# Kernel optimization log

Hardware: AMD Instinct MI355X
Metric: run time of the kernel (lower is better)

Reference implementation:

```python
import jax, jax.numpy as jnp
import numpy as np

B, T = 256, 512
V, H, L, O = 29275, 128, 2, 3


def setup_inputs() -> dict:
    key = jax.random.key(0)
    ks = jax.random.split(key, 8)
    s_emb = 1.0  # torch nn.Embedding default init is N(0,1)
    s = 1.0 / np.sqrt(H)  # torch GRU/Linear default U(-1/sqrt(H), 1/sqrt(H))
    return {
        "x": jax.random.randint(ks[0], (B, T), 0, V, dtype=jnp.int32),
        "emb": jax.random.normal(ks[1], (V, H), dtype=jnp.float32) * s_emb,
        "W_ih": jax.random.uniform(ks[2], (L, 3 * H, H), jnp.float32, -s, s),
        "W_hh": jax.random.uniform(ks[3], (L, 3 * H, H), jnp.float32, -s, s),
        "b_ih": jax.random.uniform(ks[4], (L, 3 * H), jnp.float32, -s, s),
        "b_hh": jax.random.uniform(ks[5], (L, 3 * H), jnp.float32, -s, s),
        "fc_w": jax.random.uniform(ks[6], (O, H), jnp.float32, -s, s),
        "fc_b": jax.random.uniform(ks[7], (O,), jnp.float32, -s, s),
    }


def _gru_layer(inp, Wih, Whh, bih, bhh):
    # inp: [B, T, H]. PyTorch GRU gate order: r, z, n.
    gx = jnp.einsum("bth,gh->btg", inp, Wih) + bih  # [B, T, 3H] input-side gates

    def step(h, gx_t):
        gh = h @ Whh.T + bhh  # [B, 3H]
        xr, xz, xn = jnp.split(gx_t, 3, axis=-1)
        hr, hz, hn = jnp.split(gh, 3, axis=-1)
        r = jax.nn.sigmoid(xr + hr)
        z = jax.nn.sigmoid(xz + hz)
        n = jnp.tanh(xn + r * hn)
        h_new = (1.0 - z) * n + z * h
        return h_new, h_new

    h0 = jnp.zeros((inp.shape[0], Whh.shape[1]), dtype=inp.dtype)
    _, outs = jax.lax.scan(step, h0, gx.transpose(1, 0, 2))  # [T, B, H]
    return outs.transpose(1, 0, 2)


def reference(x, emb, W_ih, W_hh, b_ih, b_hh, fc_w, fc_b):
    h = emb[x]  # [B, T, H] embedding lookup
    for l in range(L):  # small fixed layer count; dropout inactive in eval mode
        h = _gru_layer(h, W_ih[l], W_hh[l], b_ih[l], b_hh[l])
    last = jax.nn.relu(h[:, -1])  # [B, H]
    return last @ fc_w.T + fc_b  # [B, O]
```

## Files before the change

kernel.cpp:

```cpp
#include <hip/hip_runtime.h>
#include <hip/hip_bf16.h>

#define B_   256
#define T_   512
#define H_   128
#define G3_  384

#define TM   128
#define TN   128
#define TK   32
#define LDA  132

#define LOG2E_F  1.4426950408889634f
#define LOG2E2_F 2.8853900817779268f

typedef float v4f __attribute__((ext_vector_type(4)));
typedef float v2f __attribute__((ext_vector_type(2)));

__device__ __forceinline__ float fast_rcp(float x) {
    return __builtin_amdgcn_rcpf(x);
}
__device__ __forceinline__ float exp2_raw(float x) {
    return __builtin_amdgcn_exp2f(x);
}

__device__ __forceinline__ void pk_fma(v2f& acc, v2f a, v2f b) {
    asm("v_pk_fma_f32 %0, %1, %2, %0" : "+v"(acc) : "v"(a), "v"(b));
}

__device__ __forceinline__ float bfly_fold4(float v) {
    int x;
    x = __builtin_amdgcn_update_dpp(0, __float_as_int(v), 0x0B1, 0xF, 0xF, true);
    v += __int_as_float(x);
    x = __builtin_amdgcn_update_dpp(0, __float_as_int(v), 0x04E, 0xF, 0xF, true);
    v += __int_as_float(x);
    return v;
}

__device__ __forceinline__ void lds_barrier() {
    asm volatile("s_waitcnt lgkmcnt(0)" ::: "memory");
    __builtin_amdgcn_s_barrier();
    asm volatile("" ::: "memory");
}

template<bool GATHER>
__global__ __launch_bounds__(256, 2)
void gx_gemm(const float* __restrict__ X,
             const int*   __restrict__ idx,
             const float* __restrict__ emb,
             const float* __restrict__ W,
             const float* __restrict__ bias,
             const float* __restrict__ bias2,
             float*       __restrict__ gx)
{
    __shared__ __align__(16) float As[2][TK][LDA];
    __shared__ __align__(16) float Bs[2][TK][LDA];

    const int tid = threadIdx.x;
    const int tn  = tid & 15;
    const int tm  = tid >> 4;
    const int n0  = blockIdx.x * TN;
    const int m0  = blockIdx.y * TM;

    const int q  = tid & 7;
    const float* rowA[4];
    const float* rowB[4];
#pragma unroll
    for (int s = 0; s < 4; s++) {
        const int r = (tid >> 3) + 32 * s;
        rowA[s] = GATHER ? (emb + (size_t)idx[m0 + r] * H_)
                         : (X + (size_t)(m0 + r) * H_);
        rowB[s] = W + (size_t)(n0 + r) * H_;
    }

    float4 stA[4], stB[4];
    auto load_chunk = [&](int kc) {
#pragma unroll
        for (int s = 0; s < 4; s++) {
            stA[s] = *(const float4*)(rowA[s] + kc + q * 4);
            stB[s] = *(const float4*)(rowB[s] + kc + q * 4);
        }
    };
    auto store_chunk = [&](int buf) {
#pragma unroll
        for (int s = 0; s < 4; s++) {
            const int r = (tid >> 3) + 32 * s;
#pragma unroll
            for (int d = 0; d < 4; d++) {
                As[buf][q * 4 + d][r] = ((const float*)&stA[s])[d];
                Bs[buf][q * 4 + d][r] = ((const float*)&stB[s])[d];
            }
        }
    };

    float4 acc[2][2][4];
#pragma unroll
    for (int a = 0; a < 2; a++)
#pragma unroll
        for (int b = 0; b < 2; b++)
#pragma unroll
            for (int c = 0; c < 4; c++) acc[a][b][c] = make_float4(0.f, 0.f, 0.f, 0.f);

    load_chunk(0);
    store_chunk(0);
    __syncthreads();

    for (int c = 0; c < 4; c++) {
        if (c < 3) load_chunk((c + 1) * TK);
        const int buf = c & 1;
#pragma unroll 4
        for (int k = 0; k < TK; k++) {
            float4 a0 = *(const float4*)&As[buf][k][tm * 4];
            float4 a1 = *(const float4*)&As[buf][k][64 + tm * 4];
            float4 b0 = *(const float4*)&Bs[buf][k][tn * 4];
            float4 b1 = *(const float4*)&Bs[buf][k][64 + tn * 4];
            float4 av[2] = {a0, a1}, bv[2] = {b0, b1};
#pragma unroll
            for (int mg = 0; mg < 2; mg++)
#pragma unroll
                for (int mi = 0; mi < 4; mi++) {
                    const float am = ((const float*)&av[mg])[mi];
#pragma unroll
                    for (int ng = 0; ng < 2; ng++) {
                        acc[mg][ng][mi].x = fmaf(am, bv[ng].x, acc[mg][ng][mi].x);
                        acc[mg][ng][mi].y = fmaf(am, bv[ng].y, acc[mg][ng][mi].y);
                        acc[mg][ng][mi].z = fmaf(am, bv[ng].z, acc[mg][ng][mi].z);
                        acc[mg][ng][mi].w = fmaf(am, bv[ng].w, acc[mg][ng][mi].w);
                    }
                }
        }
        if (c < 3) {
            store_chunk(buf ^ 1);
            __syncthreads();
        }
    }

    float4 bb0 = *(const float4*)(bias + n0 + tn * 4);
    float4 bb1 = *(const float4*)(bias + n0 + 64 + tn * 4);
    if (n0 < 2 * H_) {
        const float4 c0 = *(const float4*)(bias2 + n0 + tn * 4);
        const float4 c1 = *(const float4*)(bias2 + n0 + 64 + tn * 4);
        bb0.x += c0.x; bb0.y += c0.y; bb0.z += c0.z; bb0.w += c0.w;
        bb1.x += c1.x; bb1.y += c1.y; bb1.z += c1.z; bb1.w += c1.w;
    }
    const float esc = (n0 < 2 * H_) ? LOG2E_F : LOG2E2_F;
#pragma unroll
    for (int mg = 0; mg < 2; mg++)
#pragma unroll
        for (int mi = 0; mi < 4; mi++) {
            const int m = m0 + mg * 64 + tm * 4 + mi;
            float* dst = gx + (size_t)m * G3_ + n0;
            float4 v0 = acc[mg][0][mi];
            v0.x = (v0.x + bb0.x) * esc; v0.y = (v0.y + bb0.y) * esc;
            v0.z = (v0.z + bb0.z) * esc; v0.w = (v0.w + bb0.w) * esc;
            float4 v1 = acc[mg][1][mi];
            v1.x = (v1.x + bb1.x) * esc; v1.y = (v1.y + bb1.y) * esc;
            v1.z = (v1.z + bb1.z) * esc; v1.w = (v1.w + bb1.w) * esc;
            *(float4*)(dst + tn * 4) = v0;
            *(float4*)(dst + 64 + tn * 4) = v1;
        }
}

template<bool STORE_H, bool FINAL>
__global__ __launch_bounds__(512)
__attribute__((amdgpu_waves_per_eu(2, 2)))
void gru_rec(const float* __restrict__ gx,
             const float* __restrict__ Whh,
             const float* __restrict__ bhh,
             float*       __restrict__ hseq,
             const float* __restrict__ fc_w,
             const float* __restrict__ fc_b,
             float*       __restrict__ out)
{
    __shared__ __align__(16) float h2[2][H_];

    const int tid = threadIdx.x;
    const int b   = blockIdx.x;
    const int jg  = tid >> 2;
    const int ks  = tid & 3;

    v2f Wr[16], Wz[16], Wn[16];
    {
        const v4f* wr = (const v4f*)(Whh + (size_t)(jg      ) * H_ + ks * 32);
        const v4f* wz = (const v4f*)(Whh + (size_t)(jg + 128) * H_ + ks * 32);
        const v4f* wn = (const v4f*)(Whh + (size_t)(jg + 256) * H_ + ks * 32);
#pragma unroll
        for (int c = 0; c < 8; c++) {
            v4f t;
            t = wr[c] * LOG2E_F;  Wr[2 * c] = t.lo; Wr[2 * c + 1] = t.hi;
            t = wz[c] * LOG2E_F;  Wz[2 * c] = t.lo; Wz[2 * c + 1] = t.hi;
            t = wn[c] * LOG2E2_F; Wn[2 * c] = t.lo; Wn[2 * c + 1] = t.hi;
        }
    }

    const float bhn = bhh[jg + 2 * H_] * LOG2E2_F;

    const float* gxb = gx + (size_t)b * T_ * G3_;
    float gr = gxb[jg], gz = gxb[jg + 128], gn = gxb[jg + 256];
    float h_old = 0.0f;

    if (tid < H_) h2[0][tid] = 0.0f;

    const int hw = ((jg >> 2) & 7) * 16 + (jg >> 5) * 4 + (jg & 3);
    const int hb = ks * 4;

    const float* gnx = gxb + G3_;
    float* hp = STORE_H ? (hseq + (size_t)b * T_ * H_ + jg) : nullptr;

    __syncthreads();

#define GRU_STEP(HIN, HOUT)                                                   \
    {                                                                         \
        const float gr2_ = gnx[jg];                                           \
        const float gz2_ = gnx[jg + 128];                                     \
        const float gn2_ = gnx[jg + 256];                                     \
        gnx += G3_;                                                           \
        v2f pr = {0.f, 0.f}, pz = {0.f, 0.f}, pn = {0.f, 0.f};                \
        _Pragma("unroll")                                                     \
        for (int c = 0; c < 8; c++) {                                         \
            v4f hv = *(const v4f*)&(HIN)[16 * c + hb];                        \
            v2f hlo = hv.lo, hhi = hv.hi;                                     \
            pk_fma(pr, hlo, Wr[2 * c]);  pk_fma(pr, hhi, Wr[2 * c + 1]);      \
            pk_fma(pz, hlo, Wz[2 * c]);  pk_fma(pz, hhi, Wz[2 * c + 1]);      \
            pk_fma(pn, hlo, Wn[2 * c]);  pk_fma(pn, hhi, Wn[2 * c + 1]);      \
        }                                                                     \
        const float p0 = bfly_fold4(pr.x + pr.y);                             \
        const float p1 = bfly_fold4(pz.x + pz.y);                             \
        const float p2 = bfly_fold4(pn.x + pn.y);                             \
        const float r_ = fast_rcp(1.0f + exp2_raw(-(gr + p0)));               \
        const float z_ = fast_rcp(1.0f + exp2_raw(-(gz + p1)));               \
        const float n_ = fmaf(-2.0f,                                          \
            fast_rcp(exp2_raw(gn + r_ * (p2 + bhn)) + 1.0f), 1.0f);           \
        h_old = fmaf(z_, h_old - n_, n_);                                     \
        if (ks == 0) {                                                        \
            (HOUT)[hw] = h_old;                                               \
            if (STORE_H) *hp = h_old;                                         \
        }                                                                     \
        if (STORE_H) hp += H_;                                                \
        gr = gr2_; gz = gz2_; gn = gn2_;                                      \
        lds_barrier();                                                        \
    }

    for (int t = 0; t < T_; t += 2) {
        GRU_STEP(h2[0], h2[1])
        GRU_STEP(h2[1], h2[0])
    }
#undef GRU_STEP

    if (FINAL) {
        if (ks == 0) h2[1][jg] = fmaxf(h_old, 0.0f);
        __syncthreads();
        if (tid < 3) {
            float acc = fc_b[tid];
            const float* fw = fc_w + tid * H_;
#pragma unroll
            for (int k = 0; k < H_; k++) acc = fmaf(h2[1][k], fw[k], acc);
            out[b * 3 + tid] = acc;
        }
    }
}

extern "C" void kernel_launch(void* const* d_in, const int* in_sizes, int n_in,
                              void* d_out, int out_size, void* d_ws, size_t ws_size,
                              hipStream_t stream)
{
    const int*   x    = (const int*)  d_in[0];
    const float* emb  = (const float*)d_in[1];
    const float* W_ih = (const float*)d_in[2];
    const float* W_hh = (const float*)d_in[3];
    const float* b_ih = (const float*)d_in[4];
    const float* b_hh = (const float*)d_in[5];
    const float* fc_w = (const float*)d_in[6];
    const float* fc_b = (const float*)d_in[7];
    float* out = (float*)d_out;

    const int M = B_ * T_;
    const size_t gx_f32 = (size_t)M * G3_ * sizeof(float);

    float* gx = (float*)d_ws;
    float* h1 = (float*)((char*)d_ws + gx_f32);

    dim3 ggx(G3_ / TN, M / TM);
    dim3 bgx(256);
    dim3 grec(B_), brec(512);

    hipLaunchKernelGGL((gx_gemm<true>), ggx, bgx, 0, stream,
                       nullptr, x, emb, W_ih, b_ih, b_hh, gx);
    hipLaunchKernelGGL((gru_rec<true, false>), grec, brec, 0, stream,
                       gx, W_hh, b_hh, h1, nullptr, nullptr, nullptr);
    hipLaunchKernelGGL((gx_gemm<false>), ggx, bgx, 0, stream,
                       h1, nullptr, nullptr, W_ih + G3_ * H_, b_ih + G3_,
                       b_hh + G3_, gx);
    hipLaunchKernelGGL((gru_rec<false, true>), grec, brec, 0, stream,
                       gx, W_hh + G3_ * H_, b_hh + G3_, nullptr, fc_w, fc_b, out);
}
```

Measured before the change: 882.2 us.

## Fuse layer-2 input projection into layer-1 recurrence using extra warps

Replaces the layer-1 recurrence kernel and the layer-2 input GEMM with a single 1024-thread kernel. Half the threads run the layer-1 recurrence, and the other half compute the layer-2 input gates from the shared hidden state one step behind, writing them back into the gx buffer in place. This removes the h1 sequence round trip through global memory and one kernel launch. The cost is doubled block size and register pressure, plus per-step barriers over twice as many waves, which may slow the serial recurrence.

```diff
diff --git a/kernel.cpp b/kernel.cpp
--- a/kernel.cpp
+++ b/kernel.cpp
@@ -159,6 +159,150 @@
             *(float4*)(dst + tn * 4) = v0;
             *(float4*)(dst + 64 + tn * 4) = v1;
         }
+}
+
+__global__ __launch_bounds__(1024)
+__attribute__((amdgpu_waves_per_eu(4, 4)))
+void gru_fused(float*       __restrict__ gx,
+               const float* __restrict__ Whh,
+               const float* __restrict__ bhh,
+               const float* __restrict__ Wih2,
+               const float* __restrict__ bih2,
+               const float* __restrict__ bhh2)
+{
+    __shared__ __align__(16) float h2[2][H_];
+
+    const int tid = threadIdx.x;
+    const int b   = blockIdx.x;
+    float* gxb = gx + (size_t)b * T_ * G3_;
+
+    if (tid < H_) h2[0][tid] = 0.0f;
+    __syncthreads();
+
+    if (tid < 512) {
+        const int jg = tid >> 2;
+        const int ks = tid & 3;
+
+        v2f Wr[16], Wz[16], Wn[16];
+        {
+            const v4f* wr = (const v4f*)(Whh + (size_t)(jg      ) * H_ + ks * 32);
+            const v4f* wz = (const v4f*)(Whh + (size_t)(jg + 128) * H_ + ks * 32);
+            const v4f* wn = (const v4f*)(Whh + (size_t)(jg + 256) * H_ + ks * 32);
+#pragma unroll
+            for (int c = 0; c < 8; c++) {
+                v4f t;
+                t = wr[c] * LOG2E_F;  Wr[2 * c] = t.lo; Wr[2 * c + 1] = t.hi;
+                t = wz[c] * LOG2E_F;  Wz[2 * c] = t.lo; Wz[2 * c + 1] = t.hi;
+                t = wn[c] * LOG2E2_F; Wn[2 * c] = t.lo; Wn[2 * c + 1] = t.hi;
+            }
+        }
+
+        const float bhn = bhh[jg + 2 * H_] * LOG2E2_F;
+        float gr = gxb[jg], gz = gxb[jg + 128], gn = gxb[jg + 256];
+        float h_old = 0.0f;
+
+        const int hw = ((jg >> 2) & 7) * 16 + (jg >> 5) * 4 + (jg & 3);
+        const int hb = ks * 4;
+        const float* gnx = gxb + G3_;
+
+#define REC_STEP(HIN, HOUT)                                                   \
+        {                                                                     \
+            const float gr2_ = gnx[jg];                                       \
+            const float gz2_ = gnx[jg + 128];                                 \
+            const float gn2_ = gnx[jg + 256];                                 \
+            gnx += G3_;                                                       \
+            v2f pr = {0.f, 0.f}, pz = {0.f, 0.f}, pn = {0.f, 0.f};            \
+            _Pragma("unroll")                                                 \
+            for (int c = 0; c < 8; c++) {                                     \
+                v4f hv = *(const v4f*)&(HIN)[16 * c + hb];                    \
+                v2f hlo = hv.lo, hhi = hv.hi;                                 \
+                pk_fma(pr, hlo, Wr[2 * c]);  pk_fma(pr, hhi, Wr[2 * c + 1]);  \
+                pk_fma(pz, hlo, Wz[2 * c]);  pk_fma(pz, hhi, Wz[2 * c + 1]);  \
+                pk_fma(pn, hlo, Wn[2 * c]);  pk_fma(pn, hhi, Wn[2 * c + 1]);  \
+            }                                                                 \
+            const float p0 = bfly_fold4(pr.x + pr.y);                         \
+            const float p1 = bfly_fold4(pz.x + pz.y);                         \
+            const float p2 = bfly_fold4(pn.x + pn.y);                         \
+            const float r_ = fast_rcp(1.0f + exp2_raw(-(gr + p0)));           \
+            const float z_ = fast_rcp(1.0f + exp2_raw(-(gz + p1)));           \
+            const float n_ = fmaf(-2.0f,                                      \
+                fast_rcp(exp2_raw(gn + r_ * (p2 + bhn)) + 1.0f), 1.0f);       \
+            h_old = fmaf(z_, h_old - n_, n_);                                 \
+            if (ks == 0) (HOUT)[hw] = h_old;                                  \
+            gr = gr2_; gz = gz2_; gn = gn2_;                                  \
+            lds_barrier();                                                    \
+        }
+
+        for (int t = 0; t < T_; t += 2) {
+            REC_STEP(h2[0], h2[1])
+            REC_STEP(h2[1], h2[0])
+        }
+#undef REC_STEP
+    } else {
+        const int t2 = tid - 512;
+        const int jq = t2 >> 2;
+        const int kq = t2 & 3;
+
+        v2f Ar[16], Az[16], An[16];
+        {
+            const v4f* ar = (const v4f*)(Wih2 + (size_t)(jq      ) * H_ + kq * 32);
+            const v4f* az = (const v4f*)(Wih2 + (size_t)(jq + 128) * H_ + kq * 32);
+            const v4f* an = (const v4f*)(Wih2 + (size_t)(jq + 256) * H_ + kq * 32);
+#pragma unroll
+            for (int c = 0; c < 8; c++) {
+                v4f t;
+                t = ar[c] * LOG2E_F;  Ar[2 * c] = t.lo; Ar[2 * c + 1] = t.hi;
+                t = az[c] * LOG2E_F;  Az[2 * c] = t.lo; Az[2 * c + 1] = t.hi;
+                t = an[c] * LOG2E2_F; An[2 * c] = t.lo; An[2 * c + 1] = t.hi;
+            }
+        }
+
+        const float br2 = (bih2[jq]          + bhh2[jq])          * LOG2E_F;
+        const float bz2 = (bih2[jq + H_]     + bhh2[jq + H_])     * LOG2E_F;
+        const float bn2 =  bih2[jq + 2 * H_]                      * LOG2E2_F;
+
+        const int qb   = kq * 4;
+        const int woff = jq + (kq - 1) * H_;
+        float* gxw = gxb - G3_;
+
+#define Q_DOT(HIN)                                                            \
+            v2f qr = {0.f, 0.f}, qz = {0.f, 0.f}, qn = {0.f, 0.f};            \
+            _Pragma("unroll")                                                 \
+            for (int c = 0; c < 8; c++) {                                     \
+                v4f hv = *(const v4f*)&(HIN)[16 * c + qb];                    \
+                v2f hlo = hv.lo, hhi = hv.hi;                                 \
+                pk_fma(qr, hlo, Ar[2 * c]);  pk_fma(qr, hhi, Ar[2 * c + 1]);  \
+                pk_fma(qz, hlo, Az[2 * c]);  pk_fma(qz, hhi, Az[2 * c + 1]);  \
+                pk_fma(qn, hlo, An[2 * c]);  pk_fma(qn, hhi, An[2 * c + 1]);  \
+            }                                                                 \
+            const float q0 = bfly_fold4(qr.x + qr.y) + br2;                   \
+            const float q1 = bfly_fold4(qz.x + qz.y) + bz2;                   \
+            const float q2 = bfly_fold4(qn.x + qn.y) + bn2;
+
+#define Q_STEP(HIN, TT)                                                       \
+        {                                                                     \
+            Q_DOT(HIN)                                                        \
+            if ((TT) > 0 && kq != 0) {                                        \
+                gxw[woff] = (kq == 1) ? q0 : ((kq == 2) ? q1 : q2);           \
+            }                                                                 \
+            gxw += G3_;                                                       \
+            lds_barrier();                                                    \
+        }
+
+        for (int t = 0; t < T_; t += 2) {
+            Q_STEP(h2[0], t)
+            Q_STEP(h2[1], t + 1)
+        }
+
+        {
+            Q_DOT(h2[0])
+            if (kq != 0) {
+                gxw[woff] = (kq == 1) ? q0 : ((kq == 2) ? q1 : q2);
+            }
+        }
+#undef Q_STEP
+#undef Q_DOT
+    }
 }
 
 template<bool STORE_H, bool FINAL>
@@ -275,22 +419,18 @@
     float* out = (float*)d_out;
 
     const int M = B_ * T_;
-    const size_t gx_f32 = (size_t)M * G3_ * sizeof(float);
 
     float* gx = (float*)d_ws;
-    float* h1 = (float*)((char*)d_ws + gx_f32);
 
     dim3 ggx(G3_ / TN, M / TM);
     dim3 bgx(256);
-    dim3 grec(B_), brec(512);
+    dim3 grec(B_);
 
     hipLaunchKernelGGL((gx_gemm<true>), ggx, bgx, 0, stream,
                        nullptr, x, emb, W_ih, b_ih, b_hh, gx);
-    hipLaunchKernelGGL((gru_rec<true, false>), grec, brec, 0, stream,
-                       gx, W_hh, b_hh, h1, nullptr, nullptr, nullptr);
-    hipLaunchKernelGGL((gx_gemm<false>), ggx, bgx, 0, stream,
-                       h1, nullptr, nullptr, W_ih + G3_ * H_, b_ih + G3_,
-                       b_hh + G3_, gx);
-    hipLaunchKernelGGL((gru_rec<false, true>), grec, brec, 0, stream,
+    hipLaunchKernelGGL(gru_fused, grec, dim3(1024), 0, stream,
+                       gx, W_hh, b_hh,
+                       W_ih + G3_ * H_, b_ih + G3_, b_hh + G3_);
+    hipLaunchKernelGGL((gru_rec<false, true>), grec, dim3(512), 0, stream,
                        gx, W_hh + G3_ * H_, b_hh + G3_, nullptr, fc_w, fc_b, out);
 }
```

Result: faster. 836.1 us (-5.2%).
